# Kernel optimization log

Hardware: AMD Instinct MI355X
Metric: run time of the kernel (lower is better)

Reference implementation:

```python
import jax, jax.numpy as jnp
import numpy as np

N_UP, N_DOWN, N_NUC, B = 16, 16, 8, 2048
EMB, TPS = 256, 32
N_ELEC = N_UP + N_DOWN


def mlp(x, w1, b1, w2, b2):
    # subnet: one hidden layer (tanh), linear output
    return jnp.tanh(x @ w1 + b1) @ w2 + b2


def _edge_indices():
    up = np.arange(N_UP)
    down = np.arange(N_UP, N_ELEC)

    def block_pairs(b):
        s, r = np.meshgrid(b, b, indexing='ij')
        m = s != r
        return s[m], r[m]

    s1, r1 = block_pairs(up)
    s2, r2 = block_pairs(down)
    senders_same = np.concatenate([s1, s2])
    receivers_same = np.concatenate([r1, r2])
    su, rd = np.meshgrid(up, down, indexing='ij')
    sd, ru = np.meshgrid(down, up, indexing='ij')
    senders_anti = np.concatenate([su.ravel(), sd.ravel()])
    receivers_anti = np.concatenate([rd.ravel(), ru.ravel()])
    senders_ne = np.repeat(np.arange(N_NUC), N_ELEC)
    receivers_ne = np.tile(np.arange(N_ELEC), N_NUC)
    return (senders_same, receivers_same, senders_anti, receivers_anti,
            senders_ne, receivers_ne)


def setup_inputs() -> dict:
    key = jax.random.key(0)
    ks = iter(jax.random.split(key, 32))

    def p(shape):
        return jax.random.normal(next(ks), shape, jnp.float32) * 0.1

    ss, rs, sa, ra, sn, rn = _edge_indices()
    inp = dict(
        electrons=p((B, N_ELEC, EMB)),
        nuclei=p((B, N_NUC, EMB)),
        feat_same=p((B, len(ss), TPS)),
        feat_anti=p((B, len(sa), TPS)),
        feat_ne=p((B, len(sn), TPS)),
        # u: per-edge-type deep-feature MLPs (TPS -> TPS)
        u_w1=p((3, TPS, TPS)), u_b1=jnp.zeros((3, TPS)),
        u_w2=p((3, TPS, TPS)), u_b2=jnp.zeros((3, TPS)),
        # w: per-edge-type message weight MLPs (TPS -> TPS)
        w_w1=p((3, TPS, TPS)), w_b1=jnp.zeros((3, TPS)),
        w_w2=p((3, TPS, TPS)), w_b2=jnp.zeros((3, TPS)),
        # h: per-edge-type sender-node MLPs (EMB -> TPS)
        h_w1=p((3, EMB, TPS)), h_b1=jnp.zeros((3, TPS)),
        h_w2=p((3, TPS, TPS)), h_b2=jnp.zeros((3, TPS)),
        # g: node update MLP (EMB + 3*TPS -> EMB), update_rule='concatenate'
        g_w1=p((EMB + 3 * TPS, EMB)), g_b1=jnp.zeros((EMB,)),
        g_w2=p((EMB, EMB)), g_b2=jnp.zeros((EMB,)),
        senders_same=jnp.asarray(ss, jnp.int32),
        receivers_same=jnp.asarray(rs, jnp.int32),
        senders_anti=jnp.asarray(sa, jnp.int32),
        receivers_anti=jnp.asarray(ra, jnp.int32),
        senders_ne=jnp.asarray(sn, jnp.int32),
        receivers_ne=jnp.asarray(rn, jnp.int32),
    )
    return inp


def reference(electrons, nuclei, feat_same, feat_anti, feat_ne,
              u_w1, u_b1, u_w2, u_b2,
              w_w1, w_b1, w_w2, w_b2,
              h_w1, h_b1, h_w2, h_b2,
              g_w1, g_b1, g_w2, g_b2,
              senders_same, receivers_same,
              senders_anti, receivers_anti,
              senders_ne, receivers_ne):
    feats = [feat_same, feat_anti, feat_ne]
    senders = [senders_same, senders_anti, senders_ne]
    receivers = [receivers_same, receivers_anti, receivers_ne]
    sender_nodes = [electrons, electrons, nuclei]
    z = []
    for t in range(3):  # fixed small set of edge types: same, anti, ne
        # deep features with two-particle residual (residual add)
        e = feats[t] + mlp(feats[t], u_w1[t], u_b1[t], u_w2[t], u_b2[t])
        we = mlp(e, w_w1[t], w_b1[t], w_w2[t], w_b2[t])              # [B, E_t, TPS]
        hx_nodes = mlp(sender_nodes[t], h_w1[t], h_b1[t], h_w2[t], h_b2[t])
        hx = hx_nodes[:, senders[t]]                                  # gather senders
        msg = we * hx
        # segment-sum over receivers into electron nodes
        zt = jnp.zeros((electrons.shape[0], N_ELEC, msg.shape[-1]), msg.dtype)
        z.append(zt.at[:, receivers[t]].add(msg))
    z_same, z_anti, z_ne = z
    # mean aggregation denominators (self_interaction=False -> self_mod=1)
    den_same = jnp.clip(jnp.concatenate(
        [jnp.full((N_UP, 1), N_UP - 1.0), jnp.full((N_DOWN, 1), N_DOWN - 1.0)]), 1.0)
    den_anti = jnp.clip(jnp.concatenate(
        [jnp.full((N_UP, 1), float(N_DOWN)), jnp.full((N_DOWN, 1), float(N_UP))]), 1.0)
    f = jnp.concatenate(
        [electrons, z_ne / N_NUC, z_same / den_same, z_anti / den_anti], axis=-1)
    updated = mlp(f, g_w1, g_b1, g_w2, g_b2)
    # one-particle residual (add)
    return electrons + updated
```

## Files before the change

kernel.cpp:

```cpp
#include <hip/hip_runtime.h>
#include <math.h>

#define NE    32
#define NN    8
#define EMB   256
#define TPS   32
#define E_SAME 480
#define E_ANTI 512
#define E_NE   256

typedef float f32x4 __attribute__((ext_vector_type(4)));
typedef short s16x8 __attribute__((ext_vector_type(8)));

__device__ __forceinline__ short f2bf(float x) {
    unsigned u = __builtin_bit_cast(unsigned, x);
    u += 0x7fffu + ((u >> 16) & 1u);
    return (short)(u >> 16);
}
__device__ __forceinline__ float bf2f(short h) {
    unsigned u = ((unsigned)(unsigned short)h) << 16;
    return __builtin_bit_cast(float, u);
}
__device__ __forceinline__ float fast_tanh(float x) {
    float e = __builtin_amdgcn_exp2f(x * 2.8853900817779268f);
    return 1.f - 2.f * __builtin_amdgcn_rcpf(e + 1.f);
}

#define WS_SHORTS 192512

__global__ void prep_weights(const float* __restrict__ u_w1, const float* __restrict__ u_w2,
                             const float* __restrict__ w_w1, const float* __restrict__ w_w2,
                             const float* __restrict__ h_w1, const float* __restrict__ g_w1,
                             const float* __restrict__ g_w2, short* __restrict__ wsb)
{
    int tile = blockIdx.x, lane = threadIdx.x;
    const float* src; int N, ks, nt, dst;
    if (tile < 24) {
        int m = tile / 6, r = tile % 6, t = r >> 1; nt = r & 1; ks = 0;
        const float* mp = (m == 0) ? u_w1 : (m == 1) ? u_w2 : (m == 2) ? w_w1 : w_w2;
        src = mp + t * 1024; N = 32; dst = m * 3072 + t * 1024 + nt * 512;
    } else if (tile < 72) {
        int i = tile - 24; int t = i >> 4, r = i & 15; nt = r >> 3; ks = r & 7;
        src = h_w1 + t * 8192; N = 32; dst = 12288 + t * 8192 + (nt * 8 + ks) * 512;
    } else if (tile < 248) {
        int i = tile - 72; nt = i / 11; ks = i - nt * 11;
        src = g_w1; N = 256; dst = 36864 + i * 512;
    } else {
        int i = tile - 248; nt = i >> 3; ks = i & 7;
        src = g_w2; N = 256; dst = 126976 + i * 512;
    }
    int kb = ks * 32 + (lane >> 4) * 8, n = nt * 16 + (lane & 15);
    s16x8 v;
    #pragma unroll
    for (int i = 0; i < 8; ++i) v[i] = f2bf(src[(size_t)(kb + i) * N + n]);
    *(s16x8*)(wsb + dst + lane * 8) = v;
}

__launch_bounds__(512, 4)
__global__ void gnn_kernel(
    const float* __restrict__ elec, const float* __restrict__ nuc,
    const float* __restrict__ fs,  const float* __restrict__ fa,  const float* __restrict__ fn,
    const float* __restrict__ u_b1, const float* __restrict__ u_b2,
    const float* __restrict__ w_b1, const float* __restrict__ w_b2,
    const float* __restrict__ h_b1, const float* __restrict__ h_w2, const float* __restrict__ h_b2,
    const float* __restrict__ g_b1, const float* __restrict__ g_b2,
    const int* __restrict__ ss, const int* __restrict__ rs,
    const int* __restrict__ sa, const int* __restrict__ ra,
    const int* __restrict__ sn, const int* __restrict__ rn,
    const short* __restrict__ wsb,
    float* __restrict__ out)
{
    __shared__ __align__(16) char smem[65440];
    short* f_s  = (short*)smem;
    float* z_s  = (float*)(smem + 23040);
    float* hx_s = (float*)(smem + 35456);
    short* H_s  = (short*)(smem + 23040);
    short* Y_s  = (short*)(smem + 44960);

    const int tid  = threadIdx.x;
    const int b    = blockIdx.x;
    const int lane = tid & 63, wv = tid >> 6;
    const int g    = lane >> 4, q = lane & 15;
    short* wb = (short*)(smem + 44960) + wv * 1280;

    for (int task = wv; task < 10; task += 8) {
        int t, mt, nt;
        if (task < 8) { t = task >> 2; mt = (task >> 1) & 1; nt = task & 1; }
        else          { t = 2; mt = 0; nt = task & 1; }
        const float* src; int row;
        if (t < 2) { row = mt * 16 + q; src = elec + ((size_t)b * NE + row) * EMB; }
        else       { row = (q < 7) ? q : 7; src = nuc + ((size_t)b * NN + row) * EMB; }
        f32x4 acc = {0.f, 0.f, 0.f, 0.f};
        #pragma unroll
        for (int ks = 0; ks < 8; ++ks) {
            int k0 = ks * 32 + g * 8;
            float4 v0 = *(const float4*)(src + k0);
            float4 v1 = *(const float4*)(src + k0 + 4);
            s16x8 a = { f2bf(v0.x), f2bf(v0.y), f2bf(v0.z), f2bf(v0.w),
                        f2bf(v1.x), f2bf(v1.y), f2bf(v1.z), f2bf(v1.w) };
            s16x8 bw = *(const s16x8*)(wsb + 12288 + t * 8192 + (nt * 8 + ks) * 512 + lane * 8);
            acc = __builtin_amdgcn_mfma_f32_16x16x32_bf16(a, bw, acc, 0, 0, 0);
            if (t == 0 && nt == 0)
                *(s16x8*)(f_s + row * 360 + k0) = a;
        }
        float bias = h_b1[t * 32 + nt * 16 + q];
        int yr = t * 32 + mt * 16 + 4 * g;
        #pragma unroll
        for (int r = 0; r < 4; ++r)
            Y_s[(yr + r) * 40 + nt * 16 + q] = f2bf(fast_tanh(acc[r] + bias));
    }
    __syncthreads();

    for (int i = tid; i < 72 * 32; i += 512) {
        int n = i >> 5, j = i & 31;
        int t = n >> 5;
        float a = h_b2[t * 32 + j];
        const float* w = h_w2 + t * 1024 + j;
        const short* yrow = Y_s + n * 40;
        #pragma unroll
        for (int k = 0; k < 32; ++k) a += bf2f(yrow[k]) * w[k * 32];
        hx_s[n * 33 + j] = a;
    }
    for (int i = tid; i < 32 * 97; i += 512) z_s[i] = 0.f;
    __syncthreads();

    short* Fb = wb;
    short* Bb = wb + 640;
    for (int t = 0; t < 3; ++t) {
        const float* ft; const int* snd; const int* rcv; int cnt, zc0;
        if (t == 0)      { ft = fs; snd = ss; rcv = rs; cnt = E_SAME; zc0 = 32; }
        else if (t == 1) { ft = fa; snd = sa; rcv = ra; cnt = E_ANTI; zc0 = 64; }
        else             { ft = fn; snd = sn; rcv = rn; cnt = E_NE;   zc0 = 0;  }
        s16x8 bu1[2], bu2[2], bw1[2], bw2[2];
        float vb1[2], vb2[2], vb3[2], vb4[2];
        #pragma unroll
        for (int nt = 0; nt < 2; ++nt) {
            int off = t * 1024 + nt * 512 + lane * 8;
            bu1[nt] = *(const s16x8*)(wsb + off);
            bu2[nt] = *(const s16x8*)(wsb + 3072 + off);
            bw1[nt] = *(const s16x8*)(wsb + 6144 + off);
            bw2[nt] = *(const s16x8*)(wsb + 9216 + off);
            int col = t * 32 + nt * 16 + q;
            vb1[nt] = u_b1[col]; vb2[nt] = u_b2[col];
            vb3[nt] = w_b1[col]; vb4[nt] = w_b2[col];
        }
        const float* hxt = hx_s + t * 32 * 33;
        int ntile = cnt >> 4;
        for (int tt = wv; tt < ntile; tt += 8) {
            int e0 = tt << 4;
            const float* fp = ft + ((size_t)b * cnt + e0 + q) * TPS + g * 8;
            float4 v0 = *(const float4*)fp;
            float4 v1 = *(const float4*)(fp + 4);
            s16x8 aF = { f2bf(v0.x), f2bf(v0.y), f2bf(v0.z), f2bf(v0.w),
                         f2bf(v1.x), f2bf(v1.y), f2bf(v1.z), f2bf(v1.w) };
            *(s16x8*)(Fb + q * 40 + g * 8) = aF;
            f32x4 z4 = {0.f, 0.f, 0.f, 0.f};
            f32x4 a0 = __builtin_amdgcn_mfma_f32_16x16x32_bf16(aF, bu1[0], z4, 0, 0, 0);
            f32x4 a1 = __builtin_amdgcn_mfma_f32_16x16x32_bf16(aF, bu1[1], z4, 0, 0, 0);
            #pragma unroll
            for (int r = 0; r < 4; ++r) {
                Bb[(4 * g + r) * 40 + q]      = f2bf(fast_tanh(a0[r] + vb1[0]));
                Bb[(4 * g + r) * 40 + 16 + q] = f2bf(fast_tanh(a1[r] + vb1[1]));
            }
            s16x8 aH = *(const s16x8*)(Bb + q * 40 + g * 8);
            a0 = __builtin_amdgcn_mfma_f32_16x16x32_bf16(aH, bu2[0], z4, 0, 0, 0);
            a1 = __builtin_amdgcn_mfma_f32_16x16x32_bf16(aH, bu2[1], z4, 0, 0, 0);
            #pragma unroll
            for (int r = 0; r < 4; ++r) {
                float fc0 = bf2f(Fb[(4 * g + r) * 40 + q]);
                float fc1 = bf2f(Fb[(4 * g + r) * 40 + 16 + q]);
                Bb[(4 * g + r) * 40 + q]      = f2bf(fc0 + a0[r] + vb2[0]);
                Bb[(4 * g + r) * 40 + 16 + q] = f2bf(fc1 + a1[r] + vb2[1]);
            }
            aH = *(const s16x8*)(Bb + q * 40 + g * 8);
            a0 = __builtin_amdgcn_mfma_f32_16x16x32_bf16(aH, bw1[0], z4, 0, 0, 0);
            a1 = __builtin_amdgcn_mfma_f32_16x16x32_bf16(aH, bw1[1], z4, 0, 0, 0);
            #pragma unroll
            for (int r = 0; r < 4; ++r) {
                Bb[(4 * g + r) * 40 + q]      = f2bf(fast_tanh(a0[r] + vb3[0]));
                Bb[(4 * g + r) * 40 + 16 + q] = f2bf(fast_tanh(a1[r] + vb3[1]));
            }
            aH = *(const s16x8*)(Bb + q * 40 + g * 8);
            a0 = __builtin_amdgcn_mfma_f32_16x16x32_bf16(aH, bw2[0], z4, 0, 0, 0);
            a1 = __builtin_amdgcn_mfma_f32_16x16x32_bf16(aH, bw2[1], z4, 0, 0, 0);
            int4 s4 = *(const int4*)(snd + e0 + 4 * g);
            int4 r4 = *(const int4*)(rcv + e0 + 4 * g);
            const int* sp = (const int*)&s4;
            const int* rp = (const int*)&r4;
            #pragma unroll
            for (int r = 0; r < 4; ++r) {
                int sv = sp[r], rv = rp[r];
                float we0 = a0[r] + vb4[0];
                float we1 = a1[r] + vb4[1];
                atomicAdd(&z_s[rv * 97 + zc0 + q],      we0 * hxt[sv * 33 + q]);
                atomicAdd(&z_s[rv * 97 + zc0 + 16 + q], we1 * hxt[sv * 33 + 16 + q]);
            }
        }
    }
    __syncthreads();

    for (int i = tid; i < 32 * 96; i += 512) {
        int r = i / 96, c = i - r * 96;
        float sc = (c < 32) ? 0.125f : ((c < 64) ? (1.f / 15.f) : (1.f / 16.f));
        f_s[r * 360 + 256 + c] = f2bf(z_s[r * 97 + c] * sc);
    }
    __syncthreads();

    for (int task = wv; task < 32; task += 8) {
        int mt = task >> 4, nt = task & 15;
        f32x4 acc = {0.f, 0.f, 0.f, 0.f};
        const short* arow = f_s + (mt * 16 + q) * 360 + g * 8;
        const short* wp = wsb + 36864 + nt * 11 * 512 + lane * 8;
        #pragma unroll
        for (int ks = 0; ks < 11; ++ks) {
            s16x8 a  = *(const s16x8*)(arow + ks * 32);
            s16x8 bw = *(const s16x8*)(wp + ks * 512);
            acc = __builtin_amdgcn_mfma_f32_16x16x32_bf16(a, bw, acc, 0, 0, 0);
        }
        float bias = g_b1[nt * 16 + q];
        #pragma unroll
        for (int r = 0; r < 4; ++r)
            H_s[(mt * 16 + 4 * g + r) * 264 + nt * 16 + q] = f2bf(fast_tanh(acc[r] + bias));
    }
    __syncthreads();

    for (int task = wv; task < 32; task += 8) {
        int mt = task >> 4, nt = task & 15;
        f32x4 acc = {0.f, 0.f, 0.f, 0.f};
        const short* arow = H_s + (mt * 16 + q) * 264 + g * 8;
        const short* wp = wsb + 126976 + nt * 8 * 512 + lane * 8;
        #pragma unroll
        for (int ks = 0; ks < 8; ++ks) {
            s16x8 a  = *(const s16x8*)(arow + ks * 32);
            s16x8 bw = *(const s16x8*)(wp + ks * 512);
            acc = __builtin_amdgcn_mfma_f32_16x16x32_bf16(a, bw, acc, 0, 0, 0);
        }
        float bias = g_b2[nt * 16 + q];
        #pragma unroll
        for (int r = 0; r < 4; ++r) {
            int row = mt * 16 + 4 * g + r, col = nt * 16 + q;
            size_t o = ((size_t)b * NE + row) * EMB + col;
            out[o] = bf2f(f_s[row * 360 + col]) + acc[r] + bias;
        }
    }
}

extern "C" void kernel_launch(void* const* d_in, const int* in_sizes, int n_in,
                              void* d_out, int out_size, void* d_ws, size_t ws_size,
                              hipStream_t stream) {
    const float* elec = (const float*)d_in[0];
    const float* nuc  = (const float*)d_in[1];
    const float* fs   = (const float*)d_in[2];
    const float* fa   = (const float*)d_in[3];
    const float* fn   = (const float*)d_in[4];
    const float* u_w1 = (const float*)d_in[5];
    const float* u_b1 = (const float*)d_in[6];
    const float* u_w2 = (const float*)d_in[7];
    const float* u_b2 = (const float*)d_in[8];
    const float* w_w1 = (const float*)d_in[9];
    const float* w_b1 = (const float*)d_in[10];
    const float* w_w2 = (const float*)d_in[11];
    const float* w_b2 = (const float*)d_in[12];
    const float* h_w1 = (const float*)d_in[13];
    const float* h_b1 = (const float*)d_in[14];
    const float* h_w2 = (const float*)d_in[15];
    const float* h_b2 = (const float*)d_in[16];
    const float* g_w1 = (const float*)d_in[17];
    const float* g_b1 = (const float*)d_in[18];
    const float* g_w2 = (const float*)d_in[19];
    const float* g_b2 = (const float*)d_in[20];
    const int* ss = (const int*)d_in[21];
    const int* rs = (const int*)d_in[22];
    const int* sa = (const int*)d_in[23];
    const int* ra = (const int*)d_in[24];
    const int* sn = (const int*)d_in[25];
    const int* rn = (const int*)d_in[26];

    short* wsb = (short*)d_ws;
    int nb = in_sizes[0] / (NE * EMB);

    prep_weights<<<376, 64, 0, stream>>>(u_w1, u_w2, w_w1, w_w2, h_w1, g_w1, g_w2, wsb);
    gnn_kernel<<<nb, 512, 0, stream>>>(elec, nuc, fs, fa, fn,
        u_b1, u_b2, w_b1, w_b2, h_b1, h_w2, h_b2, g_b1, g_b2,
        ss, rs, sa, ra, sn, rn, wsb, (float*)d_out);
}
```

Baseline: 507.6 us.

## Transpose edge MLPs to keep activations in registers via 16x16x16 MFMA chaining

```diff
diff --git a/kernel.cpp b/kernel.cpp
--- a/kernel.cpp
+++ b/kernel.cpp
@@ -1,15 +1,26 @@
 #include <hip/hip_runtime.h>
 #include <math.h>
 
-#define NE    32
-#define NN    8
-#define EMB   256
-#define TPS   32
+#define NE 32
+#define NN 8
+#define EMB 256
+#define TPS 32
 #define E_SAME 480
 #define E_ANTI 512
-#define E_NE   256
+#define E_NE 256
+
+#define AU1_OFF 0
+#define AU2_OFF 3072
+#define AW1_OFF 6144
+#define AW2_OFF 9216
+#define H1T_OFF 12288
+#define H2T_OFF 36864
+#define BIAS_OFF 39936
+#define G1_OFF 40512
+#define G2_OFF 130624
 
 typedef float f32x4 __attribute__((ext_vector_type(4)));
+typedef short s16x4 __attribute__((ext_vector_type(4)));
 typedef short s16x8 __attribute__((ext_vector_type(8)));
 
 __device__ __forceinline__ short f2bf(float x) {
@@ -25,44 +36,82 @@
     float e = __builtin_amdgcn_exp2f(x * 2.8853900817779268f);
     return 1.f - 2.f * __builtin_amdgcn_rcpf(e + 1.f);
 }
-
-#define WS_SHORTS 192512
+__device__ __forceinline__ s16x8 pack8(float4 a, float4 b) {
+    s16x8 r = { f2bf(a.x), f2bf(a.y), f2bf(a.z), f2bf(a.w),
+                f2bf(b.x), f2bf(b.y), f2bf(b.z), f2bf(b.w) };
+    return r;
+}
+__device__ __forceinline__ f32x4 mfma32(s16x8 a, s16x8 b, f32x4 c) {
+    return __builtin_amdgcn_mfma_f32_16x16x32_bf16(a, b, c, 0, 0, 0);
+}
+__device__ __forceinline__ f32x4 mfma16(s16x4 a, s16x4 b, f32x4 c) {
+    asm("v_mfma_f32_16x16x16_bf16 %0, %1, %2, %0" : "+v"(c) : "v"(a), "v"(b));
+    return c;
+}
 
 __global__ void prep_weights(const float* __restrict__ u_w1, const float* __restrict__ u_w2,
                              const float* __restrict__ w_w1, const float* __restrict__ w_w2,
-                             const float* __restrict__ h_w1, const float* __restrict__ g_w1,
-                             const float* __restrict__ g_w2, short* __restrict__ wsb)
+                             const float* __restrict__ h_w1, const float* __restrict__ h_w2,
+                             const float* __restrict__ u_b1, const float* __restrict__ u_b2,
+                             const float* __restrict__ w_b1, const float* __restrict__ w_b2,
+                             const float* __restrict__ h_b1, const float* __restrict__ h_b2,
+                             const float* __restrict__ g_w1, const float* __restrict__ g_w2,
+                             short* __restrict__ wsb)
 {
     int tile = blockIdx.x, lane = threadIdx.x;
-    const float* src; int N, ks, nt, dst;
-    if (tile < 24) {
-        int m = tile / 6, r = tile % 6, t = r >> 1; nt = r & 1; ks = 0;
-        const float* mp = (m == 0) ? u_w1 : (m == 1) ? u_w2 : (m == 2) ? w_w1 : w_w2;
-        src = mp + t * 1024; N = 32; dst = m * 3072 + t * 1024 + nt * 512;
-    } else if (tile < 72) {
-        int i = tile - 24; int t = i >> 4, r = i & 15; nt = r >> 3; ks = r & 7;
-        src = h_w1 + t * 8192; N = 32; dst = 12288 + t * 8192 + (nt * 8 + ks) * 512;
-    } else if (tile < 248) {
-        int i = tile - 72; nt = i / 11; ks = i - nt * 11;
-        src = g_w1; N = 256; dst = 36864 + i * 512;
+    int g = lane >> 4, q = lane & 15;
+    if (tile < 6) {
+        int t = tile >> 1, mt = tile & 1;
+        const float* src = u_w1 + t * 1024;
+        short* dst = wsb + AU1_OFF + tile * 512 + lane * 8;
+        #pragma unroll
+        for (int i = 0; i < 8; ++i) dst[i] = f2bf(src[(8 * g + i) * 32 + mt * 16 + q]);
+    } else if (tile < 42) {
+        int m = (tile - 6) / 12, idx = (tile - 6) % 12;
+        int mt = (idx >> 1) & 1, ks = idx & 1, t = idx >> 2;
+        const float* mp = (m == 0) ? u_w2 : (m == 1) ? w_w1 : w_w2;
+        const float* src = mp + t * 1024;
+        short* dst = wsb + AU2_OFF + m * 3072 + idx * 256 + lane * 4;
+        #pragma unroll
+        for (int i = 0; i < 4; ++i) dst[i] = f2bf(src[(ks * 16 + 4 * g + i) * 32 + mt * 16 + q]);
+    } else if (tile < 90) {
+        int idx = tile - 42;
+        int t = idx >> 4, r = idx & 15, mt = r >> 3, ks = r & 7;
+        const float* src = h_w1 + t * 8192;
+        short* dst = wsb + H1T_OFF + idx * 512 + lane * 8;
+        #pragma unroll
+        for (int i = 0; i < 8; ++i) dst[i] = f2bf(src[(ks * 32 + 8 * g + i) * 32 + mt * 16 + q]);
+    } else if (tile < 102) {
+        int idx = tile - 90;
+        int t = idx >> 2, mt = (idx >> 1) & 1, ks = idx & 1;
+        const float* src = h_w2 + t * 1024;
+        short* dst = wsb + H2T_OFF + idx * 256 + lane * 4;
+        #pragma unroll
+        for (int i = 0; i < 4; ++i) dst[i] = f2bf(src[(ks * 16 + 4 * g + i) * 32 + mt * 16 + q]);
+    } else if (tile == 102) {
+        const float* bsrc[6] = {u_b1, u_b2, w_b1, w_b2, h_b1, h_b2};
+        for (int j = lane; j < 576; j += 64)
+            wsb[BIAS_OFF + j] = f2bf(bsrc[j / 96][j % 96]);
+    } else if (tile < 279) {
+        int idx = tile - 103, nt = idx / 11, ks = idx % 11;
+        short* dst = wsb + G1_OFF + idx * 512 + lane * 8;
+        #pragma unroll
+        for (int i = 0; i < 8; ++i)
+            dst[i] = f2bf(g_w1[(size_t)(ks * 32 + 8 * g + i) * 256 + nt * 16 + q]);
     } else {
-        int i = tile - 248; nt = i >> 3; ks = i & 7;
-        src = g_w2; N = 256; dst = 126976 + i * 512;
-    }
-    int kb = ks * 32 + (lane >> 4) * 8, n = nt * 16 + (lane & 15);
-    s16x8 v;
-    #pragma unroll
-    for (int i = 0; i < 8; ++i) v[i] = f2bf(src[(size_t)(kb + i) * N + n]);
-    *(s16x8*)(wsb + dst + lane * 8) = v;
-}
-
-__launch_bounds__(512, 4)
+        int idx = tile - 279;
+        short* dst = wsb + G2_OFF + idx * 512 + lane * 8;
+        int nt = idx >> 3, ks = idx & 7;
+        #pragma unroll
+        for (int i = 0; i < 8; ++i)
+            dst[i] = f2bf(g_w2[(size_t)(ks * 32 + 8 * g + i) * 256 + nt * 16 + q]);
+    }
+}
+
+__launch_bounds__(256, 4)
 __global__ void gnn_kernel(
     const float* __restrict__ elec, const float* __restrict__ nuc,
     const float* __restrict__ fs,  const float* __restrict__ fa,  const float* __restrict__ fn,
-    const float* __restrict__ u_b1, const float* __restrict__ u_b2,
-    const float* __restrict__ w_b1, const float* __restrict__ w_b2,
-    const float* __restrict__ h_b1, const float* __restrict__ h_w2, const float* __restrict__ h_b2,
     const float* __restrict__ g_b1, const float* __restrict__ g_b2,
     const int* __restrict__ ss, const int* __restrict__ rs,
     const int* __restrict__ sa, const int* __restrict__ ra,
@@ -70,177 +119,211 @@
     const short* __restrict__ wsb,
     float* __restrict__ out)
 {
-    __shared__ __align__(16) char smem[65440];
+    __shared__ __align__(16) char smem[40384];
     short* f_s  = (short*)smem;
-    float* z_s  = (float*)(smem + 23040);
-    float* hx_s = (float*)(smem + 35456);
-    short* H_s  = (short*)(smem + 23040);
-    short* Y_s  = (short*)(smem + 44960);
+    float* z_s  = (float*)(smem + 22784);
+    short* hx_s = (short*)(smem + 35200);
+    short* H_s  = (short*)(smem + 22784);
 
     const int tid  = threadIdx.x;
     const int b    = blockIdx.x;
     const int lane = tid & 63, wv = tid >> 6;
     const int g    = lane >> 4, q = lane & 15;
-    short* wb = (short*)(smem + 44960) + wv * 1280;
-
-    for (int task = wv; task < 10; task += 8) {
-        int t, mt, nt;
-        if (task < 8) { t = task >> 2; mt = (task >> 1) & 1; nt = task & 1; }
-        else          { t = 2; mt = 0; nt = task & 1; }
-        const float* src; int row;
-        if (t < 2) { row = mt * 16 + q; src = elec + ((size_t)b * NE + row) * EMB; }
-        else       { row = (q < 7) ? q : 7; src = nuc + ((size_t)b * NN + row) * EMB; }
-        f32x4 acc = {0.f, 0.f, 0.f, 0.f};
+
+    if (wv > 0)
+        for (int i = tid - 64; i < 32 * 97; i += 192) z_s[i] = 0.f;
+
+    #pragma unroll 1
+    for (int task = wv; task < 5; task += 4) {
+        int t, nt;
+        if (task < 4) { t = task >> 1; nt = task & 1; }
+        else          { t = 2; nt = 0; }
+        const float* rowp = (t < 2) ? elec + ((size_t)b * NE + nt * 16 + q) * EMB
+                                    : nuc  + ((size_t)b * NN + (q < 8 ? q : 7)) * EMB;
+        f32x4 c0 = {0.f, 0.f, 0.f, 0.f}, c1 = {0.f, 0.f, 0.f, 0.f};
+        const short* wA = wsb + H1T_OFF + t * 16 * 512;
         #pragma unroll
         for (int ks = 0; ks < 8; ++ks) {
-            int k0 = ks * 32 + g * 8;
-            float4 v0 = *(const float4*)(src + k0);
-            float4 v1 = *(const float4*)(src + k0 + 4);
-            s16x8 a = { f2bf(v0.x), f2bf(v0.y), f2bf(v0.z), f2bf(v0.w),
-                        f2bf(v1.x), f2bf(v1.y), f2bf(v1.z), f2bf(v1.w) };
-            s16x8 bw = *(const s16x8*)(wsb + 12288 + t * 8192 + (nt * 8 + ks) * 512 + lane * 8);
-            acc = __builtin_amdgcn_mfma_f32_16x16x32_bf16(a, bw, acc, 0, 0, 0);
-            if (t == 0 && nt == 0)
-                *(s16x8*)(f_s + row * 360 + k0) = a;
-        }
-        float bias = h_b1[t * 32 + nt * 16 + q];
-        int yr = t * 32 + mt * 16 + 4 * g;
-        #pragma unroll
-        for (int r = 0; r < 4; ++r)
-            Y_s[(yr + r) * 40 + nt * 16 + q] = f2bf(fast_tanh(acc[r] + bias));
+            float4 v0 = *(const float4*)(rowp + 32 * ks + 8 * g);
+            float4 v1 = *(const float4*)(rowp + 32 * ks + 8 * g + 4);
+            s16x8 Bf = pack8(v0, v1);
+            if (t == 0) {
+                int off = (nt * 16 + q) * 356 + 32 * ks + 8 * g;
+                *(s16x4*)(f_s + off)     = __builtin_shufflevector(Bf, Bf, 0, 1, 2, 3);
+                *(s16x4*)(f_s + off + 4) = __builtin_shufflevector(Bf, Bf, 4, 5, 6, 7);
+            }
+            s16x8 a0 = *(const s16x8*)(wA + ks * 512 + lane * 8);
+            s16x8 a1 = *(const s16x8*)(wA + (8 + ks) * 512 + lane * 8);
+            c0 = mfma32(a0, Bf, c0);
+            c1 = mfma32(a1, Bf, c1);
+        }
+        s16x4 b1l = *(const s16x4*)(wsb + BIAS_OFF + (12 + t) * 32 + 4 * g);
+        s16x4 b1h = *(const s16x4*)(wsb + BIAS_OFF + (12 + t) * 32 + 16 + 4 * g);
+        s16x4 p0, p1;
+        #pragma unroll
+        for (int r = 0; r < 4; ++r) {
+            p0[r] = f2bf(fast_tanh(c0[r] + bf2f(b1l[r])));
+            p1[r] = f2bf(fast_tanh(c1[r] + bf2f(b1h[r])));
+        }
+        const short* wA2 = wsb + H2T_OFF + t * 4 * 256;
+        f32x4 d0 = {0.f, 0.f, 0.f, 0.f}, d1 = {0.f, 0.f, 0.f, 0.f};
+        d0 = mfma16(*(const s16x4*)(wA2 + 0 * 256 + lane * 4), p0, d0);
+        d0 = mfma16(*(const s16x4*)(wA2 + 1 * 256 + lane * 4), p1, d0);
+        d1 = mfma16(*(const s16x4*)(wA2 + 2 * 256 + lane * 4), p0, d1);
+        d1 = mfma16(*(const s16x4*)(wA2 + 3 * 256 + lane * 4), p1, d1);
+        if (t < 2 || q < 8) {
+            s16x4 b2l = *(const s16x4*)(wsb + BIAS_OFF + (15 + t) * 32 + 4 * g);
+            s16x4 b2h = *(const s16x4*)(wsb + BIAS_OFF + (15 + t) * 32 + 16 + 4 * g);
+            s16x4 w0, w1;
+            #pragma unroll
+            for (int r = 0; r < 4; ++r) {
+                w0[r] = f2bf(d0[r] + bf2f(b2l[r]));
+                w1[r] = f2bf(d1[r] + bf2f(b2h[r]));
+            }
+            int row = t * 32 + nt * 16 + q;
+            *(s16x4*)(hx_s + row * 36 + 4 * g)      = w0;
+            *(s16x4*)(hx_s + row * 36 + 16 + 4 * g) = w1;
+        }
     }
     __syncthreads();
 
-    for (int i = tid; i < 72 * 32; i += 512) {
-        int n = i >> 5, j = i & 31;
-        int t = n >> 5;
-        float a = h_b2[t * 32 + j];
-        const float* w = h_w2 + t * 1024 + j;
-        const short* yrow = Y_s + n * 40;
-        #pragma unroll
-        for (int k = 0; k < 32; ++k) a += bf2f(yrow[k]) * w[k * 32];
-        hx_s[n * 33 + j] = a;
-    }
-    for (int i = tid; i < 32 * 97; i += 512) z_s[i] = 0.f;
-    __syncthreads();
-
-    short* Fb = wb;
-    short* Bb = wb + 640;
+    #pragma unroll 1
     for (int t = 0; t < 3; ++t) {
         const float* ft; const int* snd; const int* rcv; int cnt, zc0;
         if (t == 0)      { ft = fs; snd = ss; rcv = rs; cnt = E_SAME; zc0 = 32; }
         else if (t == 1) { ft = fa; snd = sa; rcv = ra; cnt = E_ANTI; zc0 = 64; }
         else             { ft = fn; snd = sn; rcv = rn; cnt = E_NE;   zc0 = 0;  }
-        s16x8 bu1[2], bu2[2], bw1[2], bw2[2];
-        float vb1[2], vb2[2], vb3[2], vb4[2];
-        #pragma unroll
-        for (int nt = 0; nt < 2; ++nt) {
-            int off = t * 1024 + nt * 512 + lane * 8;
-            bu1[nt] = *(const s16x8*)(wsb + off);
-            bu2[nt] = *(const s16x8*)(wsb + 3072 + off);
-            bw1[nt] = *(const s16x8*)(wsb + 6144 + off);
-            bw2[nt] = *(const s16x8*)(wsb + 9216 + off);
-            int col = t * 32 + nt * 16 + q;
-            vb1[nt] = u_b1[col]; vb2[nt] = u_b2[col];
-            vb3[nt] = w_b1[col]; vb4[nt] = w_b2[col];
-        }
-        const float* hxt = hx_s + t * 32 * 33;
+        s16x8 Au1_0 = *(const s16x8*)(wsb + AU1_OFF + (t * 2 + 0) * 512 + lane * 8);
+        s16x8 Au1_1 = *(const s16x8*)(wsb + AU1_OFF + (t * 2 + 1) * 512 + lane * 8);
+        s16x4 Au2_[4], Aw1_[4], Aw2_[4];
+        #pragma unroll
+        for (int i = 0; i < 4; ++i) {
+            Au2_[i] = *(const s16x4*)(wsb + AU2_OFF + (t * 4 + i) * 256 + lane * 4);
+            Aw1_[i] = *(const s16x4*)(wsb + AW1_OFF + (t * 4 + i) * 256 + lane * 4);
+            Aw2_[i] = *(const s16x4*)(wsb + AW2_OFF + (t * 4 + i) * 256 + lane * 4);
+        }
+        s16x4 bb1l = *(const s16x4*)(wsb + BIAS_OFF + (0 + t) * 32 + 4 * g);
+        s16x4 bb1h = *(const s16x4*)(wsb + BIAS_OFF + (0 + t) * 32 + 16 + 4 * g);
+        s16x4 bb2l = *(const s16x4*)(wsb + BIAS_OFF + (3 + t) * 32 + 4 * g);
+        s16x4 bb2h = *(const s16x4*)(wsb + BIAS_OFF + (3 + t) * 32 + 16 + 4 * g);
+        s16x4 bb3l = *(const s16x4*)(wsb + BIAS_OFF + (6 + t) * 32 + 4 * g);
+        s16x4 bb3h = *(const s16x4*)(wsb + BIAS_OFF + (6 + t) * 32 + 16 + 4 * g);
+        s16x4 bb4l = *(const s16x4*)(wsb + BIAS_OFF + (9 + t) * 32 + 4 * g);
+        s16x4 bb4h = *(const s16x4*)(wsb + BIAS_OFF + (9 + t) * 32 + 16 + 4 * g);
+        const short* hxt = hx_s + t * 32 * 36;
         int ntile = cnt >> 4;
-        for (int tt = wv; tt < ntile; tt += 8) {
-            int e0 = tt << 4;
-            const float* fp = ft + ((size_t)b * cnt + e0 + q) * TPS + g * 8;
-            float4 v0 = *(const float4*)fp;
-            float4 v1 = *(const float4*)(fp + 4);
-            s16x8 aF = { f2bf(v0.x), f2bf(v0.y), f2bf(v0.z), f2bf(v0.w),
-                         f2bf(v1.x), f2bf(v1.y), f2bf(v1.z), f2bf(v1.w) };
-            *(s16x8*)(Fb + q * 40 + g * 8) = aF;
-            f32x4 z4 = {0.f, 0.f, 0.f, 0.f};
-            f32x4 a0 = __builtin_amdgcn_mfma_f32_16x16x32_bf16(aF, bu1[0], z4, 0, 0, 0);
-            f32x4 a1 = __builtin_amdgcn_mfma_f32_16x16x32_bf16(aF, bu1[1], z4, 0, 0, 0);
-            #pragma unroll
-            for (int r = 0; r < 4; ++r) {
-                Bb[(4 * g + r) * 40 + q]      = f2bf(fast_tanh(a0[r] + vb1[0]));
-                Bb[(4 * g + r) * 40 + 16 + q] = f2bf(fast_tanh(a1[r] + vb1[1]));
-            }
-            s16x8 aH = *(const s16x8*)(Bb + q * 40 + g * 8);
-            a0 = __builtin_amdgcn_mfma_f32_16x16x32_bf16(aH, bu2[0], z4, 0, 0, 0);
-            a1 = __builtin_amdgcn_mfma_f32_16x16x32_bf16(aH, bu2[1], z4, 0, 0, 0);
-            #pragma unroll
-            for (int r = 0; r < 4; ++r) {
-                float fc0 = bf2f(Fb[(4 * g + r) * 40 + q]);
-                float fc1 = bf2f(Fb[(4 * g + r) * 40 + 16 + q]);
-                Bb[(4 * g + r) * 40 + q]      = f2bf(fc0 + a0[r] + vb2[0]);
-                Bb[(4 * g + r) * 40 + 16 + q] = f2bf(fc1 + a1[r] + vb2[1]);
-            }
-            aH = *(const s16x8*)(Bb + q * 40 + g * 8);
-            a0 = __builtin_amdgcn_mfma_f32_16x16x32_bf16(aH, bw1[0], z4, 0, 0, 0);
-            a1 = __builtin_amdgcn_mfma_f32_16x16x32_bf16(aH, bw1[1], z4, 0, 0, 0);
-            #pragma unroll
-            for (int r = 0; r < 4; ++r) {
-                Bb[(4 * g + r) * 40 + q]      = f2bf(fast_tanh(a0[r] + vb3[0]));
-                Bb[(4 * g + r) * 40 + 16 + q] = f2bf(fast_tanh(a1[r] + vb3[1]));
-            }
-            aH = *(const s16x8*)(Bb + q * 40 + g * 8);
-            a0 = __builtin_amdgcn_mfma_f32_16x16x32_bf16(aH, bw2[0], z4, 0, 0, 0);
-            a1 = __builtin_amdgcn_mfma_f32_16x16x32_bf16(aH, bw2[1], z4, 0, 0, 0);
-            int4 s4 = *(const int4*)(snd + e0 + 4 * g);
-            int4 r4 = *(const int4*)(rcv + e0 + 4 * g);
-            const int* sp = (const int*)&s4;
-            const int* rp = (const int*)&r4;
-            #pragma unroll
-            for (int r = 0; r < 4; ++r) {
-                int sv = sp[r], rv = rp[r];
-                float we0 = a0[r] + vb4[0];
-                float we1 = a1[r] + vb4[1];
-                atomicAdd(&z_s[rv * 97 + zc0 + q],      we0 * hxt[sv * 33 + q]);
-                atomicAdd(&z_s[rv * 97 + zc0 + 16 + q], we1 * hxt[sv * 33 + 16 + q]);
-            }
+
+        const float* fp = ft + ((size_t)b * cnt + wv * 16 + q) * TPS;
+        float4 v0 = *(const float4*)(fp + 8 * g);
+        float4 v1 = *(const float4*)(fp + 8 * g + 4);
+        float4 rl = *(const float4*)(fp + 4 * g);
+        float4 rh = *(const float4*)(fp + 16 + 4 * g);
+        int se = snd[wv * 16 + q], re = rcv[wv * 16 + q];
+
+        #pragma unroll 1
+        for (int tt = wv; tt < ntile; tt += 4) {
+            int tn = tt + 4;
+            float4 n0 = {0,0,0,0}, n1 = {0,0,0,0}, nrl = {0,0,0,0}, nrh = {0,0,0,0};
+            int ns = 0, nr = 0;
+            if (tn < ntile) {
+                const float* np = ft + ((size_t)b * cnt + tn * 16 + q) * TPS;
+                n0 = *(const float4*)(np + 8 * g);
+                n1 = *(const float4*)(np + 8 * g + 4);
+                nrl = *(const float4*)(np + 4 * g);
+                nrh = *(const float4*)(np + 16 + 4 * g);
+                ns = snd[tn * 16 + q]; nr = rcv[tn * 16 + q];
+            }
+            s16x8 B32 = pack8(v0, v1);
+            f32x4 c0 = {0.f,0.f,0.f,0.f}, c1 = {0.f,0.f,0.f,0.f};
+            c0 = mfma32(Au1_0, B32, c0);
+            c1 = mfma32(Au1_1, B32, c1);
+            s16x4 p0, p1;
+            #pragma unroll
+            for (int r = 0; r < 4; ++r) {
+                p0[r] = f2bf(fast_tanh(c0[r] + bf2f(bb1l[r])));
+                p1[r] = f2bf(fast_tanh(c1[r] + bf2f(bb1h[r])));
+            }
+            f32x4 d0 = {0.f,0.f,0.f,0.f}, d1 = {0.f,0.f,0.f,0.f};
+            d0 = mfma16(Au2_[0], p0, d0); d0 = mfma16(Au2_[1], p1, d0);
+            d1 = mfma16(Au2_[2], p0, d1); d1 = mfma16(Au2_[3], p1, d1);
+            const float* rlp = (const float*)&rl; const float* rhp = (const float*)&rh;
+            #pragma unroll
+            for (int r = 0; r < 4; ++r) {
+                p0[r] = f2bf(rlp[r] + d0[r] + bf2f(bb2l[r]));
+                p1[r] = f2bf(rhp[r] + d1[r] + bf2f(bb2h[r]));
+            }
+            d0 = (f32x4){0.f,0.f,0.f,0.f}; d1 = (f32x4){0.f,0.f,0.f,0.f};
+            d0 = mfma16(Aw1_[0], p0, d0); d0 = mfma16(Aw1_[1], p1, d0);
+            d1 = mfma16(Aw1_[2], p0, d1); d1 = mfma16(Aw1_[3], p1, d1);
+            #pragma unroll
+            for (int r = 0; r < 4; ++r) {
+                p0[r] = f2bf(fast_tanh(d0[r] + bf2f(bb3l[r])));
+                p1[r] = f2bf(fast_tanh(d1[r] + bf2f(bb3h[r])));
+            }
+            d0 = (f32x4){0.f,0.f,0.f,0.f}; d1 = (f32x4){0.f,0.f,0.f,0.f};
+            d0 = mfma16(Aw2_[0], p0, d0); d0 = mfma16(Aw2_[1], p1, d0);
+            d1 = mfma16(Aw2_[2], p0, d1); d1 = mfma16(Aw2_[3], p1, d1);
+            s16x4 hlo = *(const s16x4*)(hxt + se * 36 + 4 * g);
+            s16x4 hhi = *(const s16x4*)(hxt + se * 36 + 16 + 4 * g);
+            float* zr = z_s + re * 97 + zc0 + 4 * g;
+            #pragma unroll
+            for (int r = 0; r < 4; ++r) {
+                atomicAdd(zr + r,      (d0[r] + bf2f(bb4l[r])) * bf2f(hlo[r]));
+                atomicAdd(zr + 16 + r, (d1[r] + bf2f(bb4h[r])) * bf2f(hhi[r]));
+            }
+            v0 = n0; v1 = n1; rl = nrl; rh = nrh; se = ns; re = nr;
         }
     }
     __syncthreads();
 
-    for (int i = tid; i < 32 * 96; i += 512) {
+    for (int i = tid; i < 32 * 96; i += 256) {
         int r = i / 96, c = i - r * 96;
         float sc = (c < 32) ? 0.125f : ((c < 64) ? (1.f / 15.f) : (1.f / 16.f));
-        f_s[r * 360 + 256 + c] = f2bf(z_s[r * 97 + c] * sc);
+        f_s[r * 356 + 256 + c] = f2bf(z_s[r * 97 + c] * sc);
     }
     __syncthreads();
 
-    for (int task = wv; task < 32; task += 8) {
+    #pragma unroll 1
+    for (int task = wv; task < 32; task += 4) {
         int mt = task >> 4, nt = task & 15;
         f32x4 acc = {0.f, 0.f, 0.f, 0.f};
-        const short* arow = f_s + (mt * 16 + q) * 360 + g * 8;
-        const short* wp = wsb + 36864 + nt * 11 * 512 + lane * 8;
+        const short* ar = f_s + (mt * 16 + q) * 356 + 8 * g;
+        const short* wp = wsb + G1_OFF + nt * 11 * 512 + lane * 8;
         #pragma unroll
         for (int ks = 0; ks < 11; ++ks) {
-            s16x8 a  = *(const s16x8*)(arow + ks * 32);
+            s16x4 alo = *(const s16x4*)(ar + 32 * ks);
+            s16x4 ahi = *(const s16x4*)(ar + 32 * ks + 4);
+            s16x8 a = __builtin_shufflevector(alo, ahi, 0, 1, 2, 3, 4, 5, 6, 7);
             s16x8 bw = *(const s16x8*)(wp + ks * 512);
-            acc = __builtin_amdgcn_mfma_f32_16x16x32_bf16(a, bw, acc, 0, 0, 0);
+            acc = mfma32(a, bw, acc);
         }
         float bias = g_b1[nt * 16 + q];
         #pragma unroll
         for (int r = 0; r < 4; ++r)
-            H_s[(mt * 16 + 4 * g + r) * 264 + nt * 16 + q] = f2bf(fast_tanh(acc[r] + bias));
+            H_s[(mt * 16 + 4 * g + r) * 260 + nt * 16 + q] = f2bf(fast_tanh(acc[r] + bias));
     }
     __syncthreads();
 
-    for (int task = wv; task < 32; task += 8) {
+    #pragma unroll 1
+    for (int task = wv; task < 32; task += 4) {
         int mt = task >> 4, nt = task & 15;
         f32x4 acc = {0.f, 0.f, 0.f, 0.f};
-        const short* arow = H_s + (mt * 16 + q) * 264 + g * 8;
-        const short* wp = wsb + 126976 + nt * 8 * 512 + lane * 8;
+        const short* ar = H_s + (mt * 16 + q) * 260 + 8 * g;
+        const short* wp = wsb + G2_OFF + nt * 8 * 512 + lane * 8;
         #pragma unroll
         for (int ks = 0; ks < 8; ++ks) {
-            s16x8 a  = *(const s16x8*)(arow + ks * 32);
+            s16x4 alo = *(const s16x4*)(ar + 32 * ks);
+            s16x4 ahi = *(const s16x4*)(ar + 32 * ks + 4);
+            s16x8 a = __builtin_shufflevector(alo, ahi, 0, 1, 2, 3, 4, 5, 6, 7);
             s16x8 bw = *(const s16x8*)(wp + ks * 512);
-            acc = __builtin_amdgcn_mfma_f32_16x16x32_bf16(a, bw, acc, 0, 0, 0);
+            acc = mfma32(a, bw, acc);
         }
         float bias = g_b2[nt * 16 + q];
         #pragma unroll
         for (int r = 0; r < 4; ++r) {
             int row = mt * 16 + 4 * g + r, col = nt * 16 + q;
             size_t o = ((size_t)b * NE + row) * EMB + col;
-            out[o] = bf2f(f_s[row * 360 + col]) + acc[r] + bias;
+            out[o] = bf2f(f_s[row * 356 + col]) + acc[r] + bias;
         }
     }
 }
@@ -279,8 +362,9 @@
     short* wsb = (short*)d_ws;
     int nb = in_sizes[0] / (NE * EMB);
 
-    prep_weights<<<376, 64, 0, stream>>>(u_w1, u_w2, w_w1, w_w2, h_w1, g_w1, g_w2, wsb);
-    gnn_kernel<<<nb, 512, 0, stream>>>(elec, nuc, fs, fa, fn,
-        u_b1, u_b2, w_b1, w_b2, h_b1, h_w2, h_b2, g_b1, g_b2,
-        ss, rs, sa, ra, sn, rn, wsb, (float*)d_out);
-}
+    prep_weights<<<407, 64, 0, stream>>>(u_w1, u_w2, w_w1, w_w2, h_w1, h_w2,
+                                         u_b1, u_b2, w_b1, w_b2, h_b1, h_b2,
+                                         g_w1, g_w2, wsb);
+    gnn_kernel<<<nb, 256, 0, stream>>>(elec, nuc, fs, fa, fn, g_b1, g_b2,
+                                       ss, rs, sa, ra, sn, rn, wsb, (float*)d_out);
+}
```

Measured after the change: 476.0 us. 6.2% less time.
